# Performance work log

Measured on AMD Instinct MI355X. Metric: run time of the kernel, lower is better.

The kernel has to match this reference:

```python
import jax, jax.numpy as jnp
import numpy as np

B, S, H = 1, 2048, 2048
NH, KVH, D = 32, 8, 64
G = NH // KVH  # num_key_value_groups = 4


def setup_inputs() -> dict:
    key = jax.random.key(0)
    k1, k2, k3 = jax.random.split(key, 3)
    x = jax.random.normal(k1, (B, S, H), dtype=jnp.float32)
    w_qkv = jax.random.normal(k2, ((NH + 2 * KVH) * D, H), dtype=jnp.float32) * 0.02
    w_o = jax.random.normal(k3, (H, NH * D), dtype=jnp.float32) * 0.02
    return {"x": x, "w_qkv": w_qkv, "w_o": w_o}


def _rope_cos_sin(seqlen, dim, dtype):
    inv_freq = 1.0 / (10000.0 ** (jnp.arange(0, dim, 2, dtype=jnp.float32) / dim))
    t = jnp.arange(seqlen, dtype=jnp.float32)
    freqs = jnp.outer(t, inv_freq)  # [S, D/2]
    return jnp.cos(freqs).astype(dtype), jnp.sin(freqs).astype(dtype)


def _apply_rope(x, cos, sin):
    # x: [B,S,h,D]; non-interleaved half rotation (flash-attn RotaryEmbedding)
    d2 = x.shape[-1] // 2
    x1, x2 = x[..., :d2], x[..., d2:]
    c = cos[None, :, None, :]
    s = sin[None, :, None, :]
    return jnp.concatenate([x1 * c - x2 * s, x2 * c + x1 * s], axis=-1)


def reference(x, w_qkv, w_o):
    b, s, _ = x.shape
    qkv = x @ w_qkv.T  # fused QKV proj: [B,S,(NH+2*KVH)*D]
    q, kv = jnp.split(qkv, [NH * D], axis=-1)
    q = q.reshape(b, s, NH, D)
    kv = kv.reshape(b, s, 2, KVH, D)
    cos, sin = _rope_cos_sin(s, D, x.dtype)
    q = _apply_rope(q, cos, sin)
    k = _apply_rope(kv[:, :, 0], cos, sin)
    v = kv[:, :, 1]
    # GQA: group q heads per kv head instead of repeat_interleave (same math)
    qg = q.reshape(b, s, KVH, G, D)
    scale = 1.0 / np.sqrt(D).astype(np.float32)
    scores = jnp.einsum('bskgd,btkd->bkgst', qg, k) * scale  # [B,KVH,G,S,S]
    causal = jnp.tril(jnp.ones((s, s), dtype=bool))
    scores = jnp.where(causal[None, None, None], scores, jnp.asarray(-jnp.inf, scores.dtype))
    p = jax.nn.softmax(scores, axis=-1)
    out = jnp.einsum('bkgst,btkd->bskgd', p, v).reshape(b, s, NH * D)
    return out @ w_o.T
```

## Files before the change

### kernel.cpp

```cpp
#include <hip/hip_runtime.h>


typedef __bf16 bf16_t;
typedef __attribute__((ext_vector_type(8))) __bf16 bf16x8;
typedef __attribute__((ext_vector_type(4))) __bf16 bf16x4;
typedef __attribute__((ext_vector_type(4))) float f32x4;
typedef __attribute__((ext_vector_type(2))) unsigned int u32x2;
typedef __attribute__((ext_vector_type(4))) unsigned int u32x4;

#define S_LEN 2048
#define H_DIM 2048
#define NHEAD 32
#define KVH 8
#define HD 64
#define QKV_N 3072

#define NE_PER_KH 288
#define NSPLIT_PER_KH 280
#define ENT_BYTES 16896

__global__ void cast3_kernel(const float* __restrict__ x, const float* __restrict__ wq,
                             const float* __restrict__ wo, bf16_t* __restrict__ xb,
                             bf16_t* __restrict__ wqb, bf16_t* __restrict__ wob) {
  int i = blockIdx.x * blockDim.x + threadIdx.x;
  const int n1 = S_LEN * H_DIM / 4, n2 = QKV_N * H_DIM / 4, n3 = H_DIM * H_DIM / 4;
  const float* src; bf16_t* dst; int j;
  if (i < n1)           { src = x;  dst = xb;  j = i; }
  else if (i < n1 + n2) { src = wq; dst = wqb; j = i - n1; }
  else if (i < n1 + n2 + n3) { src = wo; dst = wob; j = i - n1 - n2; }
  else return;
  float4 v = ((const float4*)src)[j];
  bf16x4 o;
  o.x = (bf16_t)v.x; o.y = (bf16_t)v.y; o.z = (bf16_t)v.z; o.w = (bf16_t)v.w;
  ((bf16x4*)dst)[j] = o;
}

__device__ __forceinline__ void async_copy16(bf16_t* lds_base, const bf16_t* g) {
  __builtin_amdgcn_global_load_lds(
      (const __attribute__((address_space(1))) unsigned int*)g,
      (__attribute__((address_space(3))) unsigned int*)lds_base, 16, 0, 0);
}

#define GBM 64
#define GBN 128

template <int EPI>
__global__ __launch_bounds__(512, 4) void gemm_sk(const bf16_t* __restrict__ A,
                                                  const bf16_t* __restrict__ B,
                                                  float* __restrict__ C,
                                                  bf16_t* __restrict__ qb,
                                                  bf16_t* __restrict__ ktp,
                                                  bf16_t* __restrict__ vt2,
                                                  int M, int N, int K) {
  __shared__ __align__(16) bf16_t smem[(2 * GBM + 2 * GBN) * 64];
  bf16_t (*As)[GBM * 64] = (bf16_t(*)[GBM * 64])smem;
  bf16_t (*Bs)[GBN * 64] = (bf16_t(*)[GBN * 64])(smem + 2 * GBM * 64);

  const int tid  = threadIdx.x;
  const int lane = tid & 63;
  const int w    = tid >> 6;
  const int wq   = w & 3;
  const int gw   = w >> 2;
  const int wm   = (wq >> 1) * 32;
  const int wn   = (wq & 1) * 64;
  const int c    = lane & 15;
  const int quad = lane >> 4;

  const int nwg = (int)(gridDim.x * gridDim.y);
  const int bid = (int)blockIdx.y * (int)gridDim.x + (int)blockIdx.x;
  const int swz = (bid & 7) * (nwg >> 3) + (bid >> 3);
  const int m0  = (swz / (int)gridDim.x) * GBM;
  const int n0  = (swz % (int)gridDim.x) * GBN;

  f32x4 acc[2][4] = {};

  const bf16_t* Ab = A + (size_t)m0 * K;
  const bf16_t* Bb = B + (size_t)n0 * K;

  const int arow = tid >> 3;
  const int akc  = (tid & 7) ^ (arow & 7);
  const int asb  = (w * 64) * 8;
  int brow[2], bkc[2], bsb[2];
#pragma unroll
  for (int i = 0; i < 2; ++i) {
    int p = i * 512 + tid;
    brow[i] = p >> 3;
    bkc[i]  = (p & 7) ^ (brow[i] & 7);
    bsb[i]  = (i * 512 + w * 64) * 8;
  }

  auto stage = [&](int buf, int k0) {
    async_copy16(&As[buf][asb], Ab + (size_t)arow * K + k0 + akc * 8);
#pragma unroll
    for (int i = 0; i < 2; ++i)
      async_copy16(&Bs[buf][bsb[i]], Bb + (size_t)brow[i] * K + k0 + bkc[i] * 8);
  };

  auto compute = [&](int buf) {
    bf16x8 af[2], bfr[4];
#pragma unroll
    for (int mt = 0; mt < 2; ++mt) {
      int row = wm + mt * 16 + c;
      af[mt] = *(const bf16x8*)&As[buf][(row * 8 + ((gw * 4 + quad) ^ (row & 7))) * 8];
    }
#pragma unroll
    for (int nt = 0; nt < 4; ++nt) {
      int rowb = wn + nt * 16 + c;
      bfr[nt] = *(const bf16x8*)&Bs[buf][(rowb * 8 + ((gw * 4 + quad) ^ (rowb & 7))) * 8];
    }
#pragma unroll
    for (int mt = 0; mt < 2; ++mt)
#pragma unroll
      for (int nt = 0; nt < 4; ++nt)
        acc[mt][nt] = __builtin_amdgcn_mfma_f32_16x16x32_bf16(af[mt], bfr[nt], acc[mt][nt], 0, 0, 0);
  };

  const int NI = K >> 6;
  stage(0, 0);
  int buf = 0;
  for (int it = 0; it < NI; ++it) {
    asm volatile("s_waitcnt vmcnt(0)" ::: "memory");
    __builtin_amdgcn_s_barrier();
    if (it + 1 < NI) stage(buf ^ 1, (it + 1) << 6);
    compute(buf);
    buf ^= 1;
  }

  __syncthreads();
  float* xch = (float*)smem;
  if (gw == 1) {
#pragma unroll
    for (int t8 = 0; t8 < 8; ++t8)
      *(f32x4*)&xch[wq * 2048 + (t8 * 64 + lane) * 4] = acc[t8 >> 2][t8 & 3];
  }
  __syncthreads();
  if (gw == 0) {
#pragma unroll
    for (int t8 = 0; t8 < 8; ++t8) {
      f32x4 o = *(const f32x4*)&xch[wq * 2048 + (t8 * 64 + lane) * 4];
      acc[t8 >> 2][t8 & 3] += o;
    }

    if (EPI == 0) {
#pragma unroll
      for (int mt = 0; mt < 2; ++mt)
#pragma unroll
        for (int nt = 0; nt < 4; ++nt)
#pragma unroll
          for (int reg = 0; reg < 4; ++reg) {
            int row = m0 + wm + mt * 16 + quad * 4 + reg;
            int col = n0 + wn + nt * 16 + c;
            C[(size_t)row * N + col] = acc[mt][nt][reg];
          }
    } else {
      const int colb = n0 + wn;
      if (colb < NHEAD * HD) {
        const int h = colb >> 6;
#pragma unroll
        for (int nt = 0; nt < 2; ++nt) {
          const int i = nt * 16 + c;
          const float invf = __expf(-(float)i * (9.210340371976184f / 32.0f));
#pragma unroll
          for (int mt = 0; mt < 2; ++mt)
#pragma unroll
            for (int reg = 0; reg < 4; ++reg) {
              const int s = m0 + wm + mt * 16 + quad * 4 + reg;
              float sn, cs;
              __sincosf((float)s * invf, &sn, &cs);
              const float x1 = acc[mt][nt][reg], x2 = acc[mt][nt + 2][reg];
              bf16_t* q = qb + (size_t)s * H_DIM + h * HD;
              q[i]      = (bf16_t)((x1 * cs - x2 * sn) * 0.125f);
              q[i + 32] = (bf16_t)((x2 * cs + x1 * sn) * 0.125f);
            }
        }
      } else if (colb < NHEAD * HD + KVH * HD) {
        const int kh = (colb - NHEAD * HD) >> 6;
#pragma unroll
        for (int nt = 0; nt < 2; ++nt) {
          const int i = nt * 16 + c;
          const float invf = __expf(-(float)i * (9.210340371976184f / 32.0f));
#pragma unroll
          for (int mt = 0; mt < 2; ++mt)
#pragma unroll
            for (int reg = 0; reg < 4; ++reg) {
              const int s = m0 + wm + mt * 16 + quad * 4 + reg;
              float sn, cs;
              __sincosf((float)s * invf, &sn, &cs);
              const float x1 = acc[mt][nt][reg], x2 = acc[mt][nt + 2][reg];
              bf16_t* kd = ktp + ((size_t)kh * S_LEN + s) * HD;
              kd[i]      = (bf16_t)(x1 * cs - x2 * sn);
              kd[i + 32] = (bf16_t)(x2 * cs + x1 * sn);
            }
        }
      } else {
        const int kh = (colb - NHEAD * HD - KVH * HD) >> 6;
#pragma unroll
        for (int nt = 0; nt < 4; ++nt) {
          const int d = nt * 16 + c;
#pragma unroll
          for (int mt = 0; mt < 2; ++mt) {
            const int sr = m0 + wm + mt * 16 + quad * 4;
            bf16x4 pv;
#pragma unroll
            for (int reg = 0; reg < 4; ++reg) pv[reg] = (bf16_t)acc[mt][nt][reg];
            *(bf16x4*)&vt2[((size_t)kh * HD + d) * S_LEN + sr] = pv;
          }
        }
      }
    }
  }
}

__global__ __launch_bounds__(256, 4) void flash_split(const bf16_t* __restrict__ qb,
                                                      const bf16_t* __restrict__ kt,
                                                      const bf16_t* __restrict__ vt2,
                                                      float* __restrict__ pbuf,
                                                      bf16_t* __restrict__ attn) {
  __shared__ __align__(16) bf16_t Ks[2][32 * 64];
  __shared__ __align__(16) bf16_t Vs[2][64 * 32];

  const int tid  = threadIdx.x;
  const int lane = tid & 63;
  const int w    = tid >> 6;
  const int e    = (int)gridDim.x - 1 - (int)blockIdx.x;
  const int kh   = e / NE_PER_KH;
  const int j    = e - kh * NE_PER_KH;

  int qt, chunk, nch;
  if (j < 8) {
    qt = j; chunk = 0; nch = 1;
  } else {
    int j2 = j - 8;
    qt = 8;
    for (;;) {
      nch = (qt + 8) >> 3;
      if (j2 < nch) { chunk = j2; break; }
      j2 -= nch; ++qt;
    }
  }
  const int T       = qt + 1;
  const int t_begin = (chunk * T) / nch;
  const int t_end   = ((chunk + 1) * T) / nch;

  const int s0    = qt * 32;
  const int h     = kh * 4 + w;
  const int c     = lane & 15;
  const int quad  = lane >> 4;

  const int idx0 = (c + (quad & 1) * 32) * 4;
  const int idx1 = idx0 + 64;
  const bool hiY = quad >= 2;

  bf16x8 qf[2][2];
#pragma unroll
  for (int rf = 0; rf < 2; ++rf)
#pragma unroll
    for (int ks = 0; ks < 2; ++ks)
      qf[rf][ks] = *(const bf16x8*)(qb + (size_t)(s0 + rf * 16 + c) * H_DIM + h * HD + ks * 32 + quad * 8);

  f32x4 acc[2][4] = {};
  float lsum[2] = {0.f, 0.f};

  const bf16_t* kbase = kt + (size_t)kh * S_LEN * HD;
  const bf16_t* vbase = vt2 + (size_t)kh * HD * S_LEN;

  const int krow = tid >> 3;
  const int kkc  = (tid & 7) ^ (krow & 7);
  const int vrow = tid >> 2;
  const int vkc  = (tid & 3) ^ ((vrow + (vrow >> 2)) & 3);
  const int sbase = w * 64 * 8;

  auto stage = [&](int buf, int tile) {
    const int t0 = tile * 32;
    async_copy16(&Ks[buf][sbase], kbase + (size_t)(t0 + krow) * HD + kkc * 8);
    async_copy16(&Vs[buf][sbase], vbase + (size_t)vrow * S_LEN + t0 + vkc * 8);
  };

  stage(0, t_begin);
  int buf = 0;
  for (int tile = t_begin; tile < t_end; ++tile) {
    const int t0 = tile * 32;
    asm volatile("s_waitcnt vmcnt(0)" ::: "memory");
    __builtin_amdgcn_s_barrier();
    if (tile + 1 < t_end) stage(buf ^ 1, tile + 1);

    const bool masked = (tile == T - 1);

    unsigned pw[2][2][2];
#pragma unroll
    for (int kt2 = 0; kt2 < 2; ++kt2) {
      bf16x8 kf0 = *(const bf16x8*)&Ks[buf][((kt2 * 16 + c) * 8 + ((quad) ^ (c & 7))) * 8];
      bf16x8 kf1 = *(const bf16x8*)&Ks[buf][((kt2 * 16 + c) * 8 + ((4 + quad) ^ (c & 7))) * 8];
#pragma unroll
      for (int rf = 0; rf < 2; ++rf) {
        f32x4 st = {};
        __builtin_amdgcn_s_setprio(1);
        st = __builtin_amdgcn_mfma_f32_16x16x32_bf16(kf0, qf[rf][0], st, 0, 0, 0);
        st = __builtin_amdgcn_mfma_f32_16x16x32_bf16(kf1, qf[rf][1], st, 0, 0, 0);
        __builtin_amdgcn_s_setprio(0);
        const int row = s0 + rf * 16 + c;
        bf16x4 pk;
#pragma unroll
        for (int reg = 0; reg < 4; ++reg) {
          const int key = t0 + kt2 * 16 + quad * 4 + reg;
          float p = __builtin_amdgcn_exp2f(fmaf(st[reg], 1.44269504f, -11.54156036f));
          if (masked && key > row) p = 0.f;
          pk[reg] = (bf16_t)p;
          lsum[rf] += p;
        }
        u32x2 pv2 = __builtin_bit_cast(u32x2, pk);
        pw[rf][kt2][0] = pv2.x;
        pw[rf][kt2][1] = pv2.y;
      }
    }

    bf16x8 vf[4];
#pragma unroll
    for (int dt = 0; dt < 4; ++dt)
      vf[dt] = *(const bf16x8*)&Vs[buf][((dt * 16 + c) * 4 + (quad ^ ((c + (c >> 2)) & 3))) * 8];

#pragma unroll
    for (int rf = 0; rf < 2; ++rf) {
      int lo, hi;
      u32x4 fwv;
      lo = __builtin_amdgcn_ds_bpermute(idx0, (int)pw[rf][0][0]);
      hi = __builtin_amdgcn_ds_bpermute(idx0, (int)pw[rf][1][0]);
      fwv.x = hiY ? (unsigned)hi : (unsigned)lo;
      lo = __builtin_amdgcn_ds_bpermute(idx0, (int)pw[rf][0][1]);
      hi = __builtin_amdgcn_ds_bpermute(idx0, (int)pw[rf][1][1]);
      fwv.y = hiY ? (unsigned)hi : (unsigned)lo;
      lo = __builtin_amdgcn_ds_bpermute(idx1, (int)pw[rf][0][0]);
      hi = __builtin_amdgcn_ds_bpermute(idx1, (int)pw[rf][1][0]);
      fwv.z = hiY ? (unsigned)hi : (unsigned)lo;
      lo = __builtin_amdgcn_ds_bpermute(idx1, (int)pw[rf][0][1]);
      hi = __builtin_amdgcn_ds_bpermute(idx1, (int)pw[rf][1][1]);
      fwv.w = hiY ? (unsigned)hi : (unsigned)lo;
      bf16x8 pa = __builtin_bit_cast(bf16x8, fwv);
      __builtin_amdgcn_s_setprio(1);
#pragma unroll
      for (int dt = 0; dt < 4; ++dt)
        acc[rf][dt] = __builtin_amdgcn_mfma_f32_16x16x32_bf16(pa, vf[dt], acc[rf][dt], 0, 0, 0);
      __builtin_amdgcn_s_setprio(0);
    }
    buf ^= 1;
  }

#pragma unroll
  for (int rf = 0; rf < 2; ++rf) {
    lsum[rf] += __shfl_xor(lsum[rf], 16);
    lsum[rf] += __shfl_xor(lsum[rf], 32);
  }

  __syncthreads();
  if (j < 8) {
    float* lbuf = (float*)&Ks[0][0] + w * 32;
#pragma unroll
    for (int rf = 0; rf < 2; ++rf) lbuf[rf * 16 + c] = lsum[rf];
    asm volatile("s_waitcnt lgkmcnt(0)" ::: "memory");
#pragma unroll
    for (int rf = 0; rf < 2; ++rf)
#pragma unroll
      for (int reg = 0; reg < 4; ++reg) {
        const float inv = 1.0f / lbuf[rf * 16 + quad * 4 + reg];
        const int row = s0 + rf * 16 + quad * 4 + reg;
#pragma unroll
        for (int dt = 0; dt < 4; ++dt)
          attn[(size_t)row * H_DIM + h * HD + dt * 16 + c] = (bf16_t)(acc[rf][dt][reg] * inv);
      }
  } else {
    const int slot = kh * NSPLIT_PER_KH + (j - 8);
    char* ent = (char*)pbuf + (size_t)slot * ENT_BYTES;
    bf16_t* eo = (bf16_t*)ent;
    float*  el = (float*)(ent + 16384);
#pragma unroll
    for (int rf = 0; rf < 2; ++rf) {
#pragma unroll
      for (int dt = 0; dt < 4; ++dt)
#pragma unroll
        for (int reg = 0; reg < 4; ++reg)
          eo[w * 2048 + (rf * 16 + quad * 4 + reg) * 64 + dt * 16 + c] = (bf16_t)acc[rf][dt][reg];
      el[w * 32 + rf * 16 + c] = lsum[rf];
    }
  }
}

__global__ __launch_bounds__(256) void flash_reduce(const float* __restrict__ pbuf,
                                                    bf16_t* __restrict__ attn) {
  const int kh = blockIdx.x / 56;
  const int qt = 8 + (blockIdx.x % 56);

  int base = 0;
  for (int q = 8; q < qt; ++q) base += (q + 8) >> 3;
  const int nch = (qt + 8) >> 3;
  base += kh * NSPLIT_PER_KH;

  const int t   = threadIdx.x;
  const int h2  = t >> 6;
  const int row = (t >> 1) & 31;
  const int dh  = t & 1;

  f32x4 o[8] = {};
  float l = 0.f;
  for (int ci = 0; ci < nch; ++ci) {
    const char* ent = (const char*)pbuf + (size_t)(base + ci) * ENT_BYTES;
    const bf16_t* p = (const bf16_t*)ent + h2 * 2048 + row * 64 + dh * 32;
#pragma unroll
    for (int jj = 0; jj < 8; ++jj) {
      bf16x4 v = ((const bf16x4*)p)[jj];
      o[jj][0] += (float)v[0]; o[jj][1] += (float)v[1];
      o[jj][2] += (float)v[2]; o[jj][3] += (float)v[3];
    }
    l += ((const float*)(ent + 16384))[h2 * 32 + row];
  }
  const float inv = 1.0f / l;
  bf16_t* dst = attn + (size_t)(qt * 32 + row) * H_DIM + (kh * 4 + h2) * 64 + dh * 32;
#pragma unroll
  for (int jj = 0; jj < 8; ++jj) {
    bf16x4 ov;
    ov[0] = (bf16_t)(o[jj][0] * inv); ov[1] = (bf16_t)(o[jj][1] * inv);
    ov[2] = (bf16_t)(o[jj][2] * inv); ov[3] = (bf16_t)(o[jj][3] * inv);
    *(bf16x4*)(dst + jj * 4) = ov;
  }
}

extern "C" void kernel_launch(void* const* d_in, const int* in_sizes, int n_in,
                              void* d_out, int out_size, void* d_ws, size_t ws_size,
                              hipStream_t stream) {
  const float* x     = (const float*)d_in[0];
  const float* w_qkv = (const float*)d_in[1];
  const float* w_o   = (const float*)d_in[2];
  float* out = (float*)d_out;

  char* ws = (char*)d_ws;
  const size_t OVERLAY = (size_t)1280 * 8320 * 4;
  bf16_t* x_bf    = (bf16_t*)ws;
  bf16_t* wqkv_bf = (bf16_t*)(ws + (size_t)S_LEN * H_DIM * 2);
  float*  pbuf    = (float*)ws;
  size_t off = OVERLAY;
  bf16_t* wo_bf   = (bf16_t*)(ws + off); off += (size_t)H_DIM * H_DIM * 2;
  bf16_t* q_bf    = (bf16_t*)(ws + off); off += (size_t)S_LEN * H_DIM * 2;
  bf16_t* k_t     = (bf16_t*)(ws + off); off += (size_t)KVH * S_LEN * HD * 2;
  bf16_t* v_t2    = (bf16_t*)(ws + off); off += (size_t)KVH * S_LEN * HD * 2;
  bf16_t* attn    = (bf16_t*)(ws + off); off += (size_t)S_LEN * H_DIM * 2;

  const int ntot = (S_LEN * H_DIM + QKV_N * H_DIM + H_DIM * H_DIM) / 4;
  cast3_kernel<<<(ntot + 255) / 256, 256, 0, stream>>>(x, w_qkv, w_o, x_bf, wqkv_bf, wo_bf);

  gemm_sk<1><<<dim3(QKV_N / GBN, S_LEN / GBM), 512, 0, stream>>>(
      x_bf, wqkv_bf, nullptr, q_bf, k_t, v_t2, S_LEN, QKV_N, H_DIM);

  flash_split<<<8 * NE_PER_KH, 256, 0, stream>>>(q_bf, k_t, v_t2, pbuf, attn);
  flash_reduce<<<8 * 56, 256, 0, stream>>>(pbuf, attn);

  gemm_sk<0><<<dim3(H_DIM / GBN, S_LEN / GBM), 512, 0, stream>>>(
      attn, wo_bf, out, nullptr, nullptr, nullptr, S_LEN, H_DIM, H_DIM);
}
```

Before: 205.0 us.

## Fuse fp32-to-bf16 casts into GEMM operand loading, drop cast kernel

Removes the separate cast kernel that converted x, w_qkv and w_o to bf16. The GEMMs now load fp32 operands into registers, convert them to bf16 and write them to LDS themselves; only the bf16 attention-output A operand still uses async global-to-LDS copies. This saves a kernel launch and a full write-then-read pass over the casted tensors. In exchange the GEMM reads twice the bytes per operand, each weight tile is re-cast by every block that uses it, and the register-staged path may hide latency less well than the async LDS copies.

```diff
diff --git a/kernel.cpp b/kernel.cpp
--- a/kernel.cpp
+++ b/kernel.cpp
@@ -19,34 +19,25 @@
 #define NSPLIT_PER_KH 280
 #define ENT_BYTES 16896
 
-__global__ void cast3_kernel(const float* __restrict__ x, const float* __restrict__ wq,
-                             const float* __restrict__ wo, bf16_t* __restrict__ xb,
-                             bf16_t* __restrict__ wqb, bf16_t* __restrict__ wob) {
-  int i = blockIdx.x * blockDim.x + threadIdx.x;
-  const int n1 = S_LEN * H_DIM / 4, n2 = QKV_N * H_DIM / 4, n3 = H_DIM * H_DIM / 4;
-  const float* src; bf16_t* dst; int j;
-  if (i < n1)           { src = x;  dst = xb;  j = i; }
-  else if (i < n1 + n2) { src = wq; dst = wqb; j = i - n1; }
-  else if (i < n1 + n2 + n3) { src = wo; dst = wob; j = i - n1 - n2; }
-  else return;
-  float4 v = ((const float4*)src)[j];
-  bf16x4 o;
-  o.x = (bf16_t)v.x; o.y = (bf16_t)v.y; o.z = (bf16_t)v.z; o.w = (bf16_t)v.w;
-  ((bf16x4*)dst)[j] = o;
-}
-
 __device__ __forceinline__ void async_copy16(bf16_t* lds_base, const bf16_t* g) {
   __builtin_amdgcn_global_load_lds(
       (const __attribute__((address_space(1))) unsigned int*)g,
       (__attribute__((address_space(3))) unsigned int*)lds_base, 16, 0, 0);
 }
 
+__device__ __forceinline__ bf16x8 cvt8(float4 a, float4 b) {
+  bf16x8 v;
+  v[0] = (bf16_t)a.x; v[1] = (bf16_t)a.y; v[2] = (bf16_t)a.z; v[3] = (bf16_t)a.w;
+  v[4] = (bf16_t)b.x; v[5] = (bf16_t)b.y; v[6] = (bf16_t)b.z; v[7] = (bf16_t)b.w;
+  return v;
+}
+
 #define GBM 64
 #define GBN 128
 
-template <int EPI>
-__global__ __launch_bounds__(512, 4) void gemm_sk(const bf16_t* __restrict__ A,
-                                                  const bf16_t* __restrict__ B,
+template <int EPI, int AF32>
+__global__ __launch_bounds__(512, 4) void gemm_sk(const void* __restrict__ Av,
+                                                  const float* __restrict__ Bf,
                                                   float* __restrict__ C,
                                                   bf16_t* __restrict__ qb,
                                                   bf16_t* __restrict__ ktp,
@@ -74,26 +65,45 @@
 
   f32x4 acc[2][4] = {};
 
-  const bf16_t* Ab = A + (size_t)m0 * K;
-  const bf16_t* Bb = B + (size_t)n0 * K;
+  const float*  Af = (const float*)Av  + (AF32 ? (size_t)m0 * K : 0);
+  const bf16_t* Ab = (const bf16_t*)Av + (AF32 ? 0 : (size_t)m0 * K);
+  const float*  Bb = Bf + (size_t)n0 * K;
 
   const int arow = tid >> 3;
   const int akc  = (tid & 7) ^ (arow & 7);
   const int asb  = (w * 64) * 8;
-  int brow[2], bkc[2], bsb[2];
+  int brow[2], bkc[2];
 #pragma unroll
   for (int i = 0; i < 2; ++i) {
     int p = i * 512 + tid;
     brow[i] = p >> 3;
     bkc[i]  = (p & 7) ^ (brow[i] & 7);
-    bsb[i]  = (i * 512 + w * 64) * 8;
-  }
-
-  auto stage = [&](int buf, int k0) {
+  }
+
+  float4 rA0, rA1, rB00, rB01, rB10, rB11;
+
+  auto ldregs = [&](int k0) {
+    if (AF32) {
+      const float* pa = Af + (size_t)arow * K + k0 + akc * 8;
+      rA0 = ((const float4*)pa)[0];
+      rA1 = ((const float4*)pa)[1];
+    }
+    const float* pb0 = Bb + (size_t)brow[0] * K + k0 + bkc[0] * 8;
+    rB00 = ((const float4*)pb0)[0];
+    rB01 = ((const float4*)pb0)[1];
+    const float* pb1 = Bb + (size_t)brow[1] * K + k0 + bkc[1] * 8;
+    rB10 = ((const float4*)pb1)[0];
+    rB11 = ((const float4*)pb1)[1];
+  };
+
+  auto wrlds = [&](int buf) {
+    if (AF32) *(bf16x8*)&As[buf][(size_t)tid * 8] = cvt8(rA0, rA1);
+    *(bf16x8*)&Bs[buf][(size_t)tid * 8]         = cvt8(rB00, rB01);
+    *(bf16x8*)&Bs[buf][(size_t)(512 + tid) * 8] = cvt8(rB10, rB11);
+  };
+
+  auto stageA_lds = [&](int buf, int k0) {
     async_copy16(&As[buf][asb], Ab + (size_t)arow * K + k0 + akc * 8);
-#pragma unroll
-    for (int i = 0; i < 2; ++i)
-      async_copy16(&Bs[buf][bsb[i]], Bb + (size_t)brow[i] * K + k0 + bkc[i] * 8);
   };
 
   auto compute = [&](int buf) {
@@ -116,12 +126,17 @@
   };
 
   const int NI = K >> 6;
-  stage(0, 0);
+  ldregs(0);
+  if (!AF32) stageA_lds(0, 0);
   int buf = 0;
   for (int it = 0; it < NI; ++it) {
-    asm volatile("s_waitcnt vmcnt(0)" ::: "memory");
+    wrlds(buf);
+    asm volatile("s_waitcnt lgkmcnt(0) vmcnt(0)" ::: "memory");
     __builtin_amdgcn_s_barrier();
-    if (it + 1 < NI) stage(buf ^ 1, (it + 1) << 6);
+    if (it + 1 < NI) {
+      ldregs((it + 1) << 6);
+      if (!AF32) stageA_lds(buf ^ 1, (it + 1) << 6);
+    }
     compute(buf);
     buf ^= 1;
   }
@@ -433,25 +448,19 @@
 
   char* ws = (char*)d_ws;
   const size_t OVERLAY = (size_t)1280 * 8320 * 4;
-  bf16_t* x_bf    = (bf16_t*)ws;
-  bf16_t* wqkv_bf = (bf16_t*)(ws + (size_t)S_LEN * H_DIM * 2);
   float*  pbuf    = (float*)ws;
   size_t off = OVERLAY;
-  bf16_t* wo_bf   = (bf16_t*)(ws + off); off += (size_t)H_DIM * H_DIM * 2;
   bf16_t* q_bf    = (bf16_t*)(ws + off); off += (size_t)S_LEN * H_DIM * 2;
   bf16_t* k_t     = (bf16_t*)(ws + off); off += (size_t)KVH * S_LEN * HD * 2;
   bf16_t* v_t2    = (bf16_t*)(ws + off); off += (size_t)KVH * S_LEN * HD * 2;
   bf16_t* attn    = (bf16_t*)(ws + off); off += (size_t)S_LEN * H_DIM * 2;
 
-  const int ntot = (S_LEN * H_DIM + QKV_N * H_DIM + H_DIM * H_DIM) / 4;
-  cast3_kernel<<<(ntot + 255) / 256, 256, 0, stream>>>(x, w_qkv, w_o, x_bf, wqkv_bf, wo_bf);
-
-  gemm_sk<1><<<dim3(QKV_N / GBN, S_LEN / GBM), 512, 0, stream>>>(
-      x_bf, wqkv_bf, nullptr, q_bf, k_t, v_t2, S_LEN, QKV_N, H_DIM);
+  gemm_sk<1, 1><<<dim3(QKV_N / GBN, S_LEN / GBM), 512, 0, stream>>>(
+      x, w_qkv, nullptr, q_bf, k_t, v_t2, S_LEN, QKV_N, H_DIM);
 
   flash_split<<<8 * NE_PER_KH, 256, 0, stream>>>(q_bf, k_t, v_t2, pbuf, attn);
   flash_reduce<<<8 * 56, 256, 0, stream>>>(pbuf, attn);
 
-  gemm_sk<0><<<dim3(H_DIM / GBN, S_LEN / GBM), 512, 0, stream>>>(
-      attn, wo_bf, out, nullptr, nullptr, nullptr, S_LEN, H_DIM, H_DIM);
-}
+  gemm_sk<0, 0><<<dim3(H_DIM / GBN, S_LEN / GBM), 512, 0, stream>>>(
+      attn, w_o, out, nullptr, nullptr, nullptr, S_LEN, H_DIM, H_DIM);
+}
```

New measurement: 267.9 us. +30.7%, slower.
